# Kernel optimization log

Measured on AMD Instinct MI355X. Metric: run time of the kernel, lower is better.

Reference implementation:

```python
import jax, jax.numpy as jnp
import numpy as np

B, C, H, W = 16, 64, 64, 64
HW = H * W            # = dim = 4096
R = 4                 # reduction_ratio
NH = 8                # head_num
EPS = 1e-5


def setup_inputs() -> dict:
    key = jax.random.key(0)
    ks = jax.random.split(key, 8)
    s = 0.02  # weight init scale
    return {
        "x": jax.random.normal(ks[0], (B, C, H, W), jnp.float32),
        "ln1_w": jnp.ones((C,), jnp.float32),
        "ln1_b": jnp.zeros((C,), jnp.float32),
        "ln2_w": jnp.ones((C,), jnp.float32),
        "ln2_b": jnp.zeros((C,), jnp.float32),
        "W_rk": jax.random.normal(ks[1], (C * R, C), jnp.float32) * s,
        "W_rv": jax.random.normal(ks[2], (C * R, C), jnp.float32) * s,
        "W_q": jax.random.normal(ks[3], (HW, HW), jnp.float32) * s,
        "W_k": jax.random.normal(ks[4], (HW // R, HW // R), jnp.float32) * s,
        "W_v": jax.random.normal(ks[5], (HW // R, HW // R), jnp.float32) * s,
        "W_o": jax.random.normal(ks[6], (HW, HW), jnp.float32) * s,
    }


def _ln(x, w, b):
    # LayerNorm over last axis
    mu = jnp.mean(x, axis=-1, keepdims=True)
    var = jnp.mean((x - mu) ** 2, axis=-1, keepdims=True)
    return (x - mu) / jnp.sqrt(var + EPS) * w + b


def reference(x, ln1_w, ln1_b, ln2_w, ln2_b, W_rk, W_rv, W_q, W_k, W_v, W_o):
    b, c, h, w = x.shape
    hw = h * w
    # ln1: LayerNorm2d == per-pixel LayerNorm over channels
    xn = _ln(x.transpose(0, 2, 3, 1), ln1_w, ln1_b)      # [B,H,W,C]
    xf = xn.reshape(b, hw, c)                            # [B,HW,C] (row-major HW)
    # K/V spatial reduction: 'a (cd r) b -> a cd (b r)'
    kv = xf.reshape(b, hw // R, R, c).transpose(0, 1, 3, 2).reshape(b, hw // R, c * R)
    k = _ln(kv @ W_rk, ln2_w, ln2_b)                     # [B,HW/R,C]
    v = _ln(kv @ W_rv, ln2_w, ln2_b)                     # [B,HW/R,C]
    # projections over the SPATIAL axis (dim = HW)
    q = xf.transpose(0, 2, 1) @ W_q                      # [B,C,HW]
    k = k.transpose(0, 2, 1) @ W_k                       # [B,C,HW/R]
    v = v.transpose(0, 2, 1) @ W_v                       # [B,C,HW/R]
    Lq = hw // NH
    Lk = (hw // R) // NH
    # split heads along spatial axis, attend over channel dim C
    qh = q.reshape(b, c, NH, Lq).transpose(0, 2, 3, 1)   # [B,h,Lq,C]
    kh = k.reshape(b, c, NH, Lk).transpose(0, 2, 3, 1)   # [B,h,Lk,C]
    vh = v.reshape(b, c, NH, Lk).transpose(0, 2, 3, 1)   # [B,h,Lk,C]
    scale = float(hw // NH) ** 0.5
    attn = jax.nn.softmax(jnp.einsum('bhqc,bhkc->bhqk', qh, kh) / scale, axis=-1)
    # dropout is identity at inference
    o = jnp.einsum('bhqk,bhkc->bhqc', attn, vh)          # [B,h,Lq,C]
    # concat_head: heads become outer blocks of the spatial axis
    o = o.transpose(0, 3, 1, 2).reshape(b, c, hw)        # [B,C,HW]
    o = o @ W_o                                          # [B,C,HW]
    return o.reshape(b, c, h, w) + x
```

## Files before the change

kernel.cpp:

```cpp
#include <hip/hip_runtime.h>

typedef unsigned short u16;
typedef unsigned int u32;
typedef __attribute__((ext_vector_type(8))) __bf16 bf16x8;
typedef __attribute__((ext_vector_type(4))) float f32x4;
typedef __attribute__((ext_vector_type(4))) unsigned int u32x4;

#define MFMA16(a, b, c) __builtin_amdgcn_mfma_f32_16x16x32_bf16((a), (b), (c), 0, 0, 0)

__device__ __forceinline__ u16 f2bf(float f) {
  unsigned u = __float_as_uint(f);
  u += 0x7FFFu + ((u >> 16) & 1u);
  return (u16)(u >> 16);
}

typedef __attribute__((address_space(1))) const unsigned char gU8;
typedef __attribute__((address_space(3))) unsigned char sU8;
__device__ __forceinline__ void gload16(const void* g, void* l) {
  __builtin_amdgcn_global_load_lds((gU8*)g, (sU8*)l, 16, 0, 0);
}

__device__ __forceinline__ void wt_body2(const float* __restrict__ W, u16* __restrict__ Wt,
                                         int K, int N, int bid, float* tile) {
  int ntn = N >> 6;
  int kt2 = bid / ntn, nt = bid % ntn;
  int t = threadIdx.x;
  const float* src = W + (size_t)kt2 * 128 * N + (size_t)nt * 64;
  f32x4 r[8];
#pragma unroll
  for (int i = 0; i < 8; ++i) {
    int idx = t + i * 256, row = idx >> 4, c4 = idx & 15;
    r[i] = *(const f32x4*)&src[(size_t)row * N + c4 * 4];
  }
#pragma unroll
  for (int i = 0; i < 8; ++i) {
    int idx = t + i * 256, row = idx >> 4, c4 = idx & 15;
#pragma unroll
    for (int j = 0; j < 4; ++j) tile[row * 65 + c4 * 4 + j] = r[i][j];
  }
  __syncthreads();
  u16* dst = Wt + (size_t)nt * 64 * K + (size_t)kt2 * 128;
  int g = t & 7, n0 = t >> 3;
#pragma unroll
  for (int i = 0; i < 2; ++i) {
    int n = n0 + i * 32;
    float v[16];
#pragma unroll
    for (int j = 0; j < 16; ++j) v[j] = tile[(g * 16 + j) * 65 + n];
    u32x4 pk0, pk1;
#pragma unroll
    for (int j = 0; j < 4; ++j) {
      pk0[j] = (u32)f2bf(v[2 * j]) | ((u32)f2bf(v[2 * j + 1]) << 16);
      pk1[j] = (u32)f2bf(v[8 + 2 * j]) | ((u32)f2bf(v[8 + 2 * j + 1]) << 16);
    }
    *(u32x4*)&dst[(size_t)n * K + g * 16] = pk0;
    *(u32x4*)&dst[(size_t)n * K + g * 16 + 8] = pk1;
  }
}

__device__ __forceinline__ void wperm_body(const float* __restrict__ Wrk, const float* __restrict__ Wrv,
                                           u16* __restrict__ Wtk, u16* __restrict__ Wtv, int bid) {
  int idx = bid * 256 + threadIdx.x;
  int cp = idx >> 8, f = idx & 255;
  int k = ((f & 63) << 2) | (f >> 6);
  Wtk[idx] = f2bf(Wrk[k * 64 + cp]);
  Wtv[idx] = f2bf(Wrv[k * 64 + cp]);
}

__device__ __forceinline__ void ln1_body(const float* __restrict__ x, const float* __restrict__ w,
                                         const float* __restrict__ bias, u16* __restrict__ xf_pc,
                                         u16* __restrict__ xfT, int bid, float* tile) {
  int b = bid >> 6, p0 = (bid & 63) << 6;
  int t = threadIdx.x;
  const float* xb = x + (size_t)b * 64 * 4096;
  f32x4 r[4];
#pragma unroll
  for (int i = 0; i < 4; ++i) {
    int idx = t + i * 256, c = idx >> 4, p4 = idx & 15;
    r[i] = *(const f32x4*)&xb[(size_t)c * 4096 + p0 + p4 * 4];
  }
#pragma unroll
  for (int i = 0; i < 4; ++i) {
    int idx = t + i * 256, c = idx >> 4, p4 = idx & 15;
#pragma unroll
    for (int j = 0; j < 4; ++j) tile[c * 65 + p4 * 4 + j] = r[i][j];
  }
  __syncthreads();
  int lane = t & 63, wvx = t >> 6;
  float gw = w[lane], gb = bias[lane];
#pragma unroll
  for (int pp = 0; pp < 16; pp += 2) {
    int p = wvx * 16 + pp;
    float v0 = tile[lane * 65 + p], v1 = tile[lane * 65 + p + 1];
    float s0 = v0, q0 = v0 * v0, s1 = v1, q1 = v1 * v1;
#pragma unroll
    for (int m = 1; m < 64; m <<= 1) {
      s0 += __shfl_xor(s0, m); q0 += __shfl_xor(q0, m);
      s1 += __shfl_xor(s1, m); q1 += __shfl_xor(q1, m);
    }
    float mu0 = s0 * (1.0f / 64.0f), var0 = q0 * (1.0f / 64.0f) - mu0 * mu0;
    float mu1 = s1 * (1.0f / 64.0f), var1 = q1 * (1.0f / 64.0f) - mu1 * mu1;
    tile[lane * 65 + p]     = (v0 - mu0) * rsqrtf(var0 + 1e-5f) * gw + gb;
    tile[lane * 65 + p + 1] = (v1 - mu1) * rsqrtf(var1 + 1e-5f) * gw + gb;
  }
  __syncthreads();
  u16* xfb = xf_pc + (size_t)b * 4096 * 64;
  u16* xtb = xfT + (size_t)b * 64 * 4096;
  int i0 = t >> 3, j8 = t & 7;
  float vc[2][8];
#pragma unroll
  for (int i = 0; i < 2; ++i)
#pragma unroll
    for (int j = 0; j < 8; ++j) vc[i][j] = tile[(j8 * 8 + j) * 65 + i0 + i * 32];
#pragma unroll
  for (int i = 0; i < 2; ++i) {
    u32x4 pk;
#pragma unroll
    for (int j = 0; j < 4; ++j)
      pk[j] = (u32)f2bf(vc[i][2 * j]) | ((u32)f2bf(vc[i][2 * j + 1]) << 16);
    *(u32x4*)&xfb[(size_t)(p0 + i0 + i * 32) * 64 + j8 * 8] = pk;
  }
  float vr[2][8];
#pragma unroll
  for (int i = 0; i < 2; ++i)
#pragma unroll
    for (int j = 0; j < 8; ++j) vr[i][j] = tile[(i0 + i * 32) * 65 + j8 * 8 + j];
#pragma unroll
  for (int i = 0; i < 2; ++i) {
    u32x4 pk;
#pragma unroll
    for (int j = 0; j < 4; ++j)
      pk[j] = (u32)f2bf(vr[i][2 * j]) | ((u32)f2bf(vr[i][2 * j + 1]) << 16);
    *(u32x4*)&xtb[(size_t)(i0 + i * 32) * 4096 + p0 + j8 * 8] = pk;
  }
}

__global__ __launch_bounds__(256) void prep_kernel(
    const float* __restrict__ W_q, u16* __restrict__ Wt_q,
    const float* __restrict__ W_o, u16* __restrict__ Wt_o,
    const float* __restrict__ W_k, u16* __restrict__ Wt_k,
    const float* __restrict__ W_v, u16* __restrict__ Wt_v,
    const float* __restrict__ W_rk, const float* __restrict__ W_rv,
    u16* __restrict__ Wt_rk, u16* __restrict__ Wt_rv,
    const float* __restrict__ x, const float* __restrict__ ln1w, const float* __restrict__ ln1b,
    u16* __restrict__ xf_pc, u16* __restrict__ xfT) {
  __shared__ float tile[128 * 65];
  int bid = blockIdx.x;
  if (bid < 2048)       wt_body2(W_q, Wt_q, 4096, 4096, bid, tile);
  else if (bid < 4096)  wt_body2(W_o, Wt_o, 4096, 4096, bid - 2048, tile);
  else if (bid < 4224)  wt_body2(W_k, Wt_k, 1024, 1024, bid - 4096, tile);
  else if (bid < 4352)  wt_body2(W_v, Wt_v, 1024, 1024, bid - 4224, tile);
  else if (bid < 4416)  wperm_body(W_rk, W_rv, Wt_rk, Wt_rv, bid - 4352);
  else                  ln1_body(x, ln1w, ln1b, xf_pc, xfT, bid - 4416, tile);
}

__global__ __launch_bounds__(256) void kv_kernel(const u16* __restrict__ xf_pc,
                                                 const u16* __restrict__ Wtk, const u16* __restrict__ Wtv,
                                                 const float* __restrict__ ln2w, const float* __restrict__ ln2b,
                                                 u16* __restrict__ kT, u16* __restrict__ vT) {
  __shared__ __align__(16) u16 As[64 * 264];
  __shared__ __align__(16) u16 Bk[64 * 264];
  __shared__ __align__(16) u16 Bv[64 * 264];
  u16* Tk = As;
  u16* Tv = As + 64 * 72;
  int b = blockIdx.x >> 4, s0 = (blockIdx.x & 15) << 6;
  int t = threadIdx.x;
  const u16* Asrc = xf_pc + (size_t)b * 4096 * 64 + (size_t)s0 * 256;
#pragma unroll
  for (int i = 0; i < 8; ++i) {
    int id = t + i * 256, row = id >> 5, c16 = id & 31;
    *(u32x4*)&As[row * 264 + c16 * 8] = *(const u32x4*)&Asrc[(size_t)row * 256 + c16 * 8];
    *(u32x4*)&Bk[row * 264 + c16 * 8] = *(const u32x4*)&Wtk[(size_t)row * 256 + c16 * 8];
    *(u32x4*)&Bv[row * 264 + c16 * 8] = *(const u32x4*)&Wtv[(size_t)row * 256 + c16 * 8];
  }
  __syncthreads();
  int lane = t & 63, wv = t >> 6, lo = lane & 15, hi = lane >> 4;
  f32x4 acck[4] = {}, accv[4] = {};
  int arow = (wv * 16 + lo) * 264 + hi * 8;
#pragma unroll
  for (int kk = 0; kk < 8; ++kk) {
    bf16x8 a = *(const bf16x8*)&As[arow + kk * 32];
#pragma unroll
    for (int nf = 0; nf < 4; ++nf) {
      bf16x8 bk = *(const bf16x8*)&Bk[(nf * 16 + lo) * 264 + kk * 32 + hi * 8];
      bf16x8 bv = *(const bf16x8*)&Bv[(nf * 16 + lo) * 264 + kk * 32 + hi * 8];
      acck[nf] = MFMA16(a, bk, acck[nf]);
      accv[nf] = MFMA16(a, bv, accv[nf]);
    }
  }
  __syncthreads();
  float w2[4], b2[4];
#pragma unroll
  for (int nf = 0; nf < 4; ++nf) { w2[nf] = ln2w[nf * 16 + lo]; b2[nf] = ln2b[nf * 16 + lo]; }
#pragma unroll
  for (int r = 0; r < 4; ++r) {
    float sk = 0.f, sk2 = 0.f, sv = 0.f, sv2 = 0.f;
#pragma unroll
    for (int nf = 0; nf < 4; ++nf) {
      float a = acck[nf][r], c = accv[nf][r];
      sk += a; sk2 += a * a; sv += c; sv2 += c * c;
    }
#pragma unroll
    for (int m = 1; m < 16; m <<= 1) {
      sk += __shfl_xor(sk, m); sk2 += __shfl_xor(sk2, m);
      sv += __shfl_xor(sv, m); sv2 += __shfl_xor(sv2, m);
    }
    float mk = sk * (1.f / 64.f), vk = sk2 * (1.f / 64.f) - mk * mk, rk = rsqrtf(vk + 1e-5f);
    float mv = sv * (1.f / 64.f), vv = sv2 * (1.f / 64.f) - mv * mv, rv = rsqrtf(vv + 1e-5f);
    int srow = wv * 16 + hi * 4 + r;
#pragma unroll
    for (int nf = 0; nf < 4; ++nf) {
      Tk[(nf * 16 + lo) * 72 + srow] = f2bf((acck[nf][r] - mk) * rk * w2[nf] + b2[nf]);
      Tv[(nf * 16 + lo) * 72 + srow] = f2bf((accv[nf][r] - mv) * rv * w2[nf] + b2[nf]);
    }
  }
  __syncthreads();
  u16* kdst = kT + (size_t)b * 64 * 1024 + s0;
  u16* vdst = vT + (size_t)b * 64 * 1024 + s0;
#pragma unroll
  for (int i = 0; i < 16; ++i) {
    int idx = t + i * 256, cp = idx >> 6, s = idx & 63;
    kdst[(size_t)cp * 1024 + s] = Tk[cp * 72 + s];
    vdst[(size_t)cp * 1024 + s] = Tv[cp * 72 + s];
  }
}

__device__ __forceinline__ void stage32(const u16* Ab, const u16* Bb, int K, int kt,
                                        u16* As, u16* Bs, int wv, int lane) {
#pragma unroll
  for (int i = 0; i < 2; ++i) {
    int cb = wv * 2 + i;
    int c = cb * 64 + lane;
    int row = c >> 2, s = c & 3;
    int scol = (s ^ (row & 3)) << 3;
    gload16(Ab + (size_t)row * K + kt * 32 + scol, As + cb * 512);
    gload16(Bb + (size_t)row * K + kt * 32 + scol, Bs + cb * 512);
  }
}

__device__ __forceinline__ void compute32(const u16* As, const u16* Bs, f32x4 acc[4][4],
                                          int wm, int wn, int lo, int hi) {
  int slot = (hi ^ (lo & 3)) << 3;
  bf16x8 a[4], bb[4];
#pragma unroll
  for (int i = 0; i < 4; ++i) {
    a[i]  = *(const bf16x8*)&As[(wm + i * 16 + lo) * 32 + slot];
    bb[i] = *(const bf16x8*)&Bs[(wn + i * 16 + lo) * 32 + slot];
  }
#pragma unroll
  for (int mi = 0; mi < 4; ++mi)
#pragma unroll
    for (int ni = 0; ni < 4; ++ni)
      acc[mi][ni] = MFMA16(a[mi], bb[ni], acc[mi][ni]);
}

template <int EPI>
__device__ void gemm_body(const u16* __restrict__ A, const u16* __restrict__ Bm,
                          u16* __restrict__ Cc, int N, int K, int chunkStride,
                          int mt, int nt, int koff, int nk, u16* lds) {
  int t = threadIdx.x, lane = t & 63, wv = t >> 6;
  int wm = (wv >> 1) * 64, wn = (wv & 1) * 64;
  int lo = lane & 15, hi = lane >> 4;
  f32x4 acc[4][4] = {};
  const u16* Ab = A + (size_t)mt * 128 * K + koff;
  const u16* Bb = Bm + (size_t)nt * 128 * K + koff;
  u16* bufs[3] = {lds, lds + 8192, lds + 16384};
  stage32(Ab, Bb, K, 0, bufs[0], bufs[0] + 4096, wv, lane);
  stage32(Ab, Bb, K, 1, bufs[1], bufs[1] + 4096, wv, lane);
  for (int kt = 0; kt < nk; ++kt) {
    if (kt + 1 < nk) asm volatile("s_waitcnt vmcnt(4)" ::: "memory");
    else             asm volatile("s_waitcnt vmcnt(0)" ::: "memory");
    __builtin_amdgcn_s_barrier();
    __builtin_amdgcn_sched_barrier(0);
    if (kt + 2 < nk) {
      u16* nb = bufs[(kt + 2) % 3];
      stage32(Ab, Bb, K, kt + 2, nb, nb + 4096, wv, lane);
    }
    u16* cb = bufs[kt % 3];
    compute32(cb, cb + 4096, acc, wm, wn, lo, hi);
  }
#pragma unroll
  for (int mi = 0; mi < 4; ++mi)
#pragma unroll
    for (int ni = 0; ni < 4; ++ni)
#pragma unroll
      for (int r = 0; r < 4; ++r) {
        int m = mt * 128 + wm + mi * 16 + hi * 4 + r;
        int n = nt * 128 + wn + ni * 16 + lo;
        float v = acc[mi][ni][r];
        if constexpr (EPI == 0) {
          Cc[(size_t)m * N + n] = f2bf(v);
        } else {
          Cc[(size_t)(n >> 6) * chunkStride + (size_t)m * 64 + (n & 63)] = f2bf(v);
        }
      }
}

__global__ __launch_bounds__(256, 3) void qkv_kernel(
    const u16* __restrict__ Wt_q, const u16* __restrict__ xfT, u16* __restrict__ q_t,
    const u16* __restrict__ Wt_k, const u16* __restrict__ k_lnT, u16* __restrict__ kproj,
    const u16* __restrict__ v_lnT, const u16* __restrict__ Wt_v, u16* __restrict__ vproj) {
  __shared__ __align__(16) u16 lds[24576];
  int bid = blockIdx.x;
  if (bid < 1024) {
    int log = (bid & 7) * 128 + (bid >> 3);
    int kh = log >> 8, tile = log & 255, mt = tile >> 3, nt = tile & 7;
    gemm_body<1>(Wt_q, xfT, q_t + (size_t)kh * 4194304, 1024, 4096, 4096 * 64,
                 mt, nt, kh * 1024, 32, lds);
  } else if (bid < 1088) {
    int id = bid - 1024;
    gemm_body<1>(Wt_k, k_lnT, kproj, 1024, 1024, 1024 * 64, id >> 3, id & 7, 0, 32, lds);
  } else {
    int id = bid - 1088;
    gemm_body<0>(v_lnT, Wt_v, vproj, 1024, 1024, 0, id >> 3, id & 7, 0, 32, lds);
  }
}

__global__ __launch_bounds__(256, 3) void ogemm_kernel(const u16* __restrict__ o2,
                                                       const u16* __restrict__ Wt_o,
                                                       u16* __restrict__ o_part) {
  __shared__ __align__(16) u16 lds[24576];
  int bid = blockIdx.x;
  int log = (bid & 7) * 64 + (bid >> 3);
  int kh = log >> 8, tile = log & 255, mt = tile >> 5, nt = tile & 31;
  gemm_body<0>(o2, Wt_o, o_part + (size_t)kh * 4194304, 4096, 4096, 0,
               mt, nt, kh * 2048, 64, lds);
}

__global__ __launch_bounds__(256) void oreduce_kernel(const float* __restrict__ x,
                                                      const u16* __restrict__ p0,
                                                      const u16* __restrict__ p1,
                                                      float* __restrict__ out) {
  size_t base = ((size_t)blockIdx.x * 256 + threadIdx.x) * 8;
  u32x4 a = *(const u32x4*)&p0[base];
  u32x4 b = *(const u32x4*)&p1[base];
  f32x4 x0 = *(const f32x4*)&x[base];
  f32x4 x1 = *(const f32x4*)&x[base + 4];
  float r[8];
#pragma unroll
  for (int j = 0; j < 4; ++j) {
    r[2 * j]     = __uint_as_float(a[j] << 16) + __uint_as_float(b[j] << 16);
    r[2 * j + 1] = __uint_as_float(a[j] & 0xFFFF0000u) + __uint_as_float(b[j] & 0xFFFF0000u);
  }
  f32x4 o0, o1;
#pragma unroll
  for (int j = 0; j < 4; ++j) { o0[j] = r[j] + x0[j]; o1[j] = r[4 + j] + x1[j]; }
  *(f32x4*)&out[base] = o0;
  *(f32x4*)&out[base + 4] = o1;
}

__global__ __launch_bounds__(256) void attn_kernel(const u16* __restrict__ qp, const u16* __restrict__ kp,
                                                   const u16* __restrict__ vp, u16* __restrict__ o2) {
  __shared__ __align__(16) u16 Qs[128 * 72];
  __shared__ __align__(16) u16 Ks[128 * 72];
  __shared__ __align__(16) u16 Vs[64 * 136];
  __shared__ __align__(16) u16 Ps[128 * 136];
  int qt = blockIdx.x & 3, h = (blockIdx.x >> 2) & 7, b = blockIdx.x >> 5;
  int t = threadIdx.x, lane = t & 63, wv = t >> 6;
  int lo = lane & 15, hi = lane >> 4;
  const u16* qsrc = qp + (size_t)b * 262144 + (size_t)(h * 512 + qt * 128) * 64;
  const u16* ksrc = kp + (size_t)b * 1024 * 64 + (size_t)(h * 128) * 64;
  const u16* vsrc = vp + (size_t)b * 64 * 1024 + h * 128;
#pragma unroll
  for (int i = 0; i < 4; ++i) {
    int id = t + i * 256, row = id >> 3, c8 = id & 7;
    size_t goff = (size_t)row * 64 + c8 * 8;
    float f[8] = {0.f, 0.f, 0.f, 0.f, 0.f, 0.f, 0.f, 0.f};
#pragma unroll
    for (int kh = 0; kh < 4; ++kh) {
      u32x4 pk = *(const u32x4*)&qsrc[(size_t)kh * 4194304 + goff];
#pragma unroll
      for (int j = 0; j < 4; ++j) {
        f[2 * j]     += __uint_as_float(pk[j] << 16);
        f[2 * j + 1] += __uint_as_float(pk[j] & 0xFFFF0000u);
      }
    }
    u32x4 pko;
#pragma unroll
    for (int j = 0; j < 4; ++j) pko[j] = (u32)f2bf(f[2 * j]) | ((u32)f2bf(f[2 * j + 1]) << 16);
    *(u32x4*)&Qs[row * 72 + c8 * 8] = pko;
  }
#pragma unroll
  for (int i = 0; i < 4; ++i) {
    int id = t + i * 256;
    int row = id >> 3, c16 = id & 7;
    *(u32x4*)&Ks[row * 72 + c16 * 8] = *(const u32x4*)&ksrc[(size_t)row * 64 + c16 * 8];
    int vrow = id >> 4, v16 = id & 15;
    *(u32x4*)&Vs[vrow * 136 + v16 * 8] = *(const u32x4*)&vsrc[(size_t)vrow * 1024 + v16 * 8];
  }
  __syncthreads();
  f32x4 s[2][8] = {};
#pragma unroll
  for (int kk = 0; kk < 2; ++kk) {
    bf16x8 a0 = *(const bf16x8*)&Qs[(wv * 32 + lo) * 72 + kk * 32 + hi * 8];
    bf16x8 a1 = *(const bf16x8*)&Qs[(wv * 32 + 16 + lo) * 72 + kk * 32 + hi * 8];
#pragma unroll
    for (int ni = 0; ni < 8; ++ni) {
      bf16x8 bb = *(const bf16x8*)&Ks[(ni * 16 + lo) * 72 + kk * 32 + hi * 8];
      s[0][ni] = MFMA16(a0, bb, s[0][ni]);
      s[1][ni] = MFMA16(a1, bb, s[1][ni]);
    }
  }
  const float inv_scale = 0.044194173824159216f;
#pragma unroll
  for (int mi = 0; mi < 2; ++mi)
#pragma unroll
    for (int ni = 0; ni < 8; ++ni) s[mi][ni] *= inv_scale;
#pragma unroll
  for (int mi = 0; mi < 2; ++mi) {
#pragma unroll
    for (int r = 0; r < 4; ++r) {
      float mx = -1e30f;
#pragma unroll
      for (int ni = 0; ni < 8; ++ni) mx = fmaxf(mx, s[mi][ni][r]);
#pragma unroll
      for (int m = 1; m < 16; m <<= 1) mx = fmaxf(mx, __shfl_xor(mx, m));
      float p[8], sum = 0.f;
#pragma unroll
      for (int ni = 0; ni < 8; ++ni) { p[ni] = __expf(s[mi][ni][r] - mx); sum += p[ni]; }
#pragma unroll
      for (int m = 1; m < 16; m <<= 1) sum += __shfl_xor(sum, m);
      float rs = 1.0f / sum;
      int row = wv * 32 + mi * 16 + hi * 4 + r;
#pragma unroll
      for (int ni = 0; ni < 8; ++ni) Ps[row * 136 + ni * 16 + lo] = f2bf(p[ni] * rs);
    }
  }
  __syncthreads();
  f32x4 o[4][2] = {};
#pragma unroll
  for (int kk = 0; kk < 4; ++kk) {
    bf16x8 b0 = *(const bf16x8*)&Ps[(wv * 32 + lo) * 136 + kk * 32 + hi * 8];
    bf16x8 b1 = *(const bf16x8*)&Ps[(wv * 32 + 16 + lo) * 136 + kk * 32 + hi * 8];
#pragma unroll
    for (int mi = 0; mi < 4; ++mi) {
      bf16x8 a = *(const bf16x8*)&Vs[(mi * 16 + lo) * 136 + kk * 32 + hi * 8];
      o[mi][0] = MFMA16(a, b0, o[mi][0]);
      o[mi][1] = MFMA16(a, b1, o[mi][1]);
    }
  }
  u16* od = o2 + (size_t)b * 64 * 4096 + h * 512 + qt * 128;
#pragma unroll
  for (int mi = 0; mi < 4; ++mi)
#pragma unroll
    for (int ni = 0; ni < 2; ++ni)
#pragma unroll
      for (int r = 0; r < 4; ++r) {
        int c = mi * 16 + hi * 4 + r;
        int lq = wv * 32 + ni * 16 + lo;
        od[(size_t)c * 4096 + lq] = f2bf(o[mi][ni][r]);
      }
}

extern "C" void kernel_launch(void* const* d_in, const int* in_sizes, int n_in,
                              void* d_out, int out_size, void* d_ws, size_t ws_size,
                              hipStream_t stream) {
  (void)in_sizes; (void)n_in; (void)out_size; (void)ws_size;
  const float* x    = (const float*)d_in[0];
  const float* ln1w = (const float*)d_in[1];
  const float* ln1b = (const float*)d_in[2];
  const float* ln2w = (const float*)d_in[3];
  const float* ln2b = (const float*)d_in[4];
  const float* W_rk = (const float*)d_in[5];
  const float* W_rv = (const float*)d_in[6];
  const float* W_q  = (const float*)d_in[7];
  const float* W_k  = (const float*)d_in[8];
  const float* W_v  = (const float*)d_in[9];
  const float* W_o  = (const float*)d_in[10];

  char* ws = (char*)d_ws;
  size_t off = 0;
  auto alloc = [&](size_t bytes) { char* p = ws + off; off += bytes; return p; };
  u16* Wt_q  = (u16*)alloc(4096ull * 4096 * 2);
  u16* Wt_o  = (u16*)alloc(4096ull * 4096 * 2);
  u16* Wt_k  = (u16*)alloc(1024ull * 1024 * 2);
  u16* Wt_v  = (u16*)alloc(1024ull * 1024 * 2);
  u16* Wt_rk = (u16*)alloc(64ull * 256 * 2);
  u16* Wt_rv = (u16*)alloc(64ull * 256 * 2);
  u16* xf_pc = (u16*)alloc(16ull * 4096 * 64 * 2);
  u16* xfT   = (u16*)alloc(16ull * 64 * 4096 * 2);
  u16* k_lnT = (u16*)alloc(16ull * 64 * 1024 * 2);
  u16* v_lnT = (u16*)alloc(16ull * 64 * 1024 * 2);
  u16* q_t   = (u16*)alloc(4ull * 16 * 4096 * 64 * 2);
  u16* kproj = (u16*)alloc(16ull * 1024 * 64 * 2);
  u16* vproj = (u16*)alloc(16ull * 64 * 1024 * 2);
  u16* o2     = xfT;
  u16* o_part = Wt_q;

  prep_kernel<<<5440, 256, 0, stream>>>(W_q, Wt_q, W_o, Wt_o, W_k, Wt_k, W_v, Wt_v,
                                        W_rk, W_rv, Wt_rk, Wt_rv, x, ln1w, ln1b, xf_pc, xfT);
  kv_kernel<<<256, 256, 0, stream>>>(xf_pc, Wt_rk, Wt_rv, ln2w, ln2b, k_lnT, v_lnT);
  qkv_kernel<<<1152, 256, 0, stream>>>(Wt_q, xfT, q_t, Wt_k, k_lnT, kproj, v_lnT, Wt_v, vproj);
  attn_kernel<<<512, 256, 0, stream>>>(q_t, kproj, vproj, o2);
  ogemm_kernel<<<512, 256, 0, stream>>>(o2, Wt_o, o_part);
  oreduce_kernel<<<2048, 256, 0, stream>>>(x, o_part, o_part + 4194304, (float*)d_out);
}
```

Measured before the change: 211.6 us.

## Redistribute weight transpose/convert work into later kernels to overlap with GEMMs

```diff
diff --git a/kernel.cpp b/kernel.cpp
--- a/kernel.cpp
+++ b/kernel.cpp
@@ -137,9 +137,6 @@
 
 __global__ __launch_bounds__(256) void prep_kernel(
     const float* __restrict__ W_q, u16* __restrict__ Wt_q,
-    const float* __restrict__ W_o, u16* __restrict__ Wt_o,
-    const float* __restrict__ W_k, u16* __restrict__ Wt_k,
-    const float* __restrict__ W_v, u16* __restrict__ Wt_v,
     const float* __restrict__ W_rk, const float* __restrict__ W_rv,
     u16* __restrict__ Wt_rk, u16* __restrict__ Wt_rv,
     const float* __restrict__ x, const float* __restrict__ ln1w, const float* __restrict__ ln1b,
@@ -147,23 +144,29 @@
   __shared__ float tile[128 * 65];
   int bid = blockIdx.x;
   if (bid < 2048)       wt_body2(W_q, Wt_q, 4096, 4096, bid, tile);
-  else if (bid < 4096)  wt_body2(W_o, Wt_o, 4096, 4096, bid - 2048, tile);
-  else if (bid < 4224)  wt_body2(W_k, Wt_k, 1024, 1024, bid - 4096, tile);
-  else if (bid < 4352)  wt_body2(W_v, Wt_v, 1024, 1024, bid - 4224, tile);
-  else if (bid < 4416)  wperm_body(W_rk, W_rv, Wt_rk, Wt_rv, bid - 4352);
-  else                  ln1_body(x, ln1w, ln1b, xf_pc, xfT, bid - 4416, tile);
+  else if (bid < 2112)  wperm_body(W_rk, W_rv, Wt_rk, Wt_rv, bid - 2048);
+  else                  ln1_body(x, ln1w, ln1b, xf_pc, xfT, bid - 2112, tile);
 }
 
 __global__ __launch_bounds__(256) void kv_kernel(const u16* __restrict__ xf_pc,
                                                  const u16* __restrict__ Wtk, const u16* __restrict__ Wtv,
                                                  const float* __restrict__ ln2w, const float* __restrict__ ln2b,
-                                                 u16* __restrict__ kT, u16* __restrict__ vT) {
+                                                 u16* __restrict__ kT, u16* __restrict__ vT,
+                                                 const float* __restrict__ W_k, u16* __restrict__ Wt_k,
+                                                 const float* __restrict__ W_v, u16* __restrict__ Wt_v) {
   __shared__ __align__(16) u16 As[64 * 264];
   __shared__ __align__(16) u16 Bk[64 * 264];
   __shared__ __align__(16) u16 Bv[64 * 264];
+  int bid0 = blockIdx.x;
+  if (bid0 >= 256) {
+    int id = bid0 - 256;
+    if (id < 128) wt_body2(W_k, Wt_k, 1024, 1024, id, (float*)As);
+    else          wt_body2(W_v, Wt_v, 1024, 1024, id - 128, (float*)As);
+    return;
+  }
   u16* Tk = As;
   u16* Tv = As + 64 * 72;
-  int b = blockIdx.x >> 4, s0 = (blockIdx.x & 15) << 6;
+  int b = bid0 >> 4, s0 = (bid0 & 15) << 6;
   int t = threadIdx.x;
   const u16* Asrc = xf_pc + (size_t)b * 4096 * 64 + (size_t)s0 * 256;
 #pragma unroll
@@ -299,7 +302,8 @@
 __global__ __launch_bounds__(256, 3) void qkv_kernel(
     const u16* __restrict__ Wt_q, const u16* __restrict__ xfT, u16* __restrict__ q_t,
     const u16* __restrict__ Wt_k, const u16* __restrict__ k_lnT, u16* __restrict__ kproj,
-    const u16* __restrict__ v_lnT, const u16* __restrict__ Wt_v, u16* __restrict__ vproj) {
+    const u16* __restrict__ v_lnT, const u16* __restrict__ Wt_v, u16* __restrict__ vproj,
+    const float* __restrict__ W_o, u16* __restrict__ Wt_o) {
   __shared__ __align__(16) u16 lds[24576];
   int bid = blockIdx.x;
   if (bid < 1024) {
@@ -310,9 +314,11 @@
   } else if (bid < 1088) {
     int id = bid - 1024;
     gemm_body<1>(Wt_k, k_lnT, kproj, 1024, 1024, 1024 * 64, id >> 3, id & 7, 0, 32, lds);
-  } else {
+  } else if (bid < 1152) {
     int id = bid - 1088;
     gemm_body<0>(v_lnT, Wt_v, vproj, 1024, 1024, 0, id >> 3, id & 7, 0, 32, lds);
+  } else {
+    wt_body2(W_o, Wt_o, 4096, 4096, bid - 1152, (float*)lds);
   }
 }
 
@@ -487,10 +493,12 @@
   u16* o2     = xfT;
   u16* o_part = Wt_q;
 
-  prep_kernel<<<5440, 256, 0, stream>>>(W_q, Wt_q, W_o, Wt_o, W_k, Wt_k, W_v, Wt_v,
-                                        W_rk, W_rv, Wt_rk, Wt_rv, x, ln1w, ln1b, xf_pc, xfT);
-  kv_kernel<<<256, 256, 0, stream>>>(xf_pc, Wt_rk, Wt_rv, ln2w, ln2b, k_lnT, v_lnT);
-  qkv_kernel<<<1152, 256, 0, stream>>>(Wt_q, xfT, q_t, Wt_k, k_lnT, kproj, v_lnT, Wt_v, vproj);
+  prep_kernel<<<3136, 256, 0, stream>>>(W_q, Wt_q, W_rk, W_rv, Wt_rk, Wt_rv,
+                                        x, ln1w, ln1b, xf_pc, xfT);
+  kv_kernel<<<512, 256, 0, stream>>>(xf_pc, Wt_rk, Wt_rv, ln2w, ln2b, k_lnT, v_lnT,
+                                     W_k, Wt_k, W_v, Wt_v);
+  qkv_kernel<<<3200, 256, 0, stream>>>(Wt_q, xfT, q_t, Wt_k, k_lnT, kproj, v_lnT, Wt_v, vproj,
+                                       W_o, Wt_o);
   attn_kernel<<<512, 256, 0, stream>>>(q_t, kproj, vproj, o2);
   ogemm_kernel<<<512, 256, 0, stream>>>(o2, Wt_o, o_part);
   oreduce_kernel<<<2048, 256, 0, stream>>>(x, o_part, o_part + 4194304, (float*)d_out);
```

New measurement: 210.8 us. About the same (-0.3%).

## Remove split-K from Q and output GEMMs, fuse residual into epilogue

Applied to the files above, without the earlier changes.

```diff
diff --git a/kernel.cpp b/kernel.cpp
--- a/kernel.cpp
+++ b/kernel.cpp
@@ -256,14 +256,14 @@
 
 template <int EPI>
 __device__ void gemm_body(const u16* __restrict__ A, const u16* __restrict__ Bm,
-                          u16* __restrict__ Cc, int N, int K, int chunkStride,
-                          int mt, int nt, int koff, int nk, u16* lds) {
+                          void* __restrict__ Cc, const float* __restrict__ resid,
+                          int N, int K, int chunkStride, int mt, int nt, int nk, u16* lds) {
   int t = threadIdx.x, lane = t & 63, wv = t >> 6;
   int wm = (wv >> 1) * 64, wn = (wv & 1) * 64;
   int lo = lane & 15, hi = lane >> 4;
   f32x4 acc[4][4] = {};
-  const u16* Ab = A + (size_t)mt * 128 * K + koff;
-  const u16* Bb = Bm + (size_t)nt * 128 * K + koff;
+  const u16* Ab = A + (size_t)mt * 128 * K;
+  const u16* Bb = Bm + (size_t)nt * 128 * K;
   u16* bufs[3] = {lds, lds + 8192, lds + 16384};
   stage32(Ab, Bb, K, 0, bufs[0], bufs[0] + 4096, wv, lane);
   stage32(Ab, Bb, K, 1, bufs[1], bufs[1] + 4096, wv, lane);
@@ -289,9 +289,12 @@
         int n = nt * 128 + wn + ni * 16 + lo;
         float v = acc[mi][ni][r];
         if constexpr (EPI == 0) {
-          Cc[(size_t)m * N + n] = f2bf(v);
+          ((u16*)Cc)[(size_t)m * N + n] = f2bf(v);
+        } else if constexpr (EPI == 1) {
+          ((u16*)Cc)[(size_t)(n >> 6) * chunkStride + (size_t)m * 64 + (n & 63)] = f2bf(v);
         } else {
-          Cc[(size_t)(n >> 6) * chunkStride + (size_t)m * 64 + (n & 63)] = f2bf(v);
+          size_t ad = (size_t)m * N + n;
+          ((float*)Cc)[ad] = v + resid[ad];
         }
       }
 }
@@ -302,51 +305,24 @@
     const u16* __restrict__ v_lnT, const u16* __restrict__ Wt_v, u16* __restrict__ vproj) {
   __shared__ __align__(16) u16 lds[24576];
   int bid = blockIdx.x;
-  if (bid < 1024) {
-    int log = (bid & 7) * 128 + (bid >> 3);
-    int kh = log >> 8, tile = log & 255, mt = tile >> 3, nt = tile & 7;
-    gemm_body<1>(Wt_q, xfT, q_t + (size_t)kh * 4194304, 1024, 4096, 4096 * 64,
-                 mt, nt, kh * 1024, 32, lds);
-  } else if (bid < 1088) {
-    int id = bid - 1024;
-    gemm_body<1>(Wt_k, k_lnT, kproj, 1024, 1024, 1024 * 64, id >> 3, id & 7, 0, 32, lds);
+  if (bid < 256) {
+    gemm_body<1>(Wt_q, xfT, q_t, nullptr, 1024, 4096, 4096 * 64, bid >> 3, bid & 7, 128, lds);
+  } else if (bid < 320) {
+    int id = bid - 256;
+    gemm_body<1>(Wt_k, k_lnT, kproj, nullptr, 1024, 1024, 1024 * 64, id >> 3, id & 7, 32, lds);
   } else {
-    int id = bid - 1088;
-    gemm_body<0>(v_lnT, Wt_v, vproj, 1024, 1024, 0, id >> 3, id & 7, 0, 32, lds);
+    int id = bid - 320;
+    gemm_body<0>(v_lnT, Wt_v, vproj, nullptr, 1024, 1024, 0, id >> 3, id & 7, 32, lds);
   }
 }
 
 __global__ __launch_bounds__(256, 3) void ogemm_kernel(const u16* __restrict__ o2,
                                                        const u16* __restrict__ Wt_o,
-                                                       u16* __restrict__ o_part) {
+                                                       float* __restrict__ out,
+                                                       const float* __restrict__ x) {
   __shared__ __align__(16) u16 lds[24576];
   int bid = blockIdx.x;
-  int log = (bid & 7) * 64 + (bid >> 3);
-  int kh = log >> 8, tile = log & 255, mt = tile >> 5, nt = tile & 31;
-  gemm_body<0>(o2, Wt_o, o_part + (size_t)kh * 4194304, 4096, 4096, 0,
-               mt, nt, kh * 2048, 64, lds);
-}
-
-__global__ __launch_bounds__(256) void oreduce_kernel(const float* __restrict__ x,
-                                                      const u16* __restrict__ p0,
-                                                      const u16* __restrict__ p1,
-                                                      float* __restrict__ out) {
-  size_t base = ((size_t)blockIdx.x * 256 + threadIdx.x) * 8;
-  u32x4 a = *(const u32x4*)&p0[base];
-  u32x4 b = *(const u32x4*)&p1[base];
-  f32x4 x0 = *(const f32x4*)&x[base];
-  f32x4 x1 = *(const f32x4*)&x[base + 4];
-  float r[8];
-#pragma unroll
-  for (int j = 0; j < 4; ++j) {
-    r[2 * j]     = __uint_as_float(a[j] << 16) + __uint_as_float(b[j] << 16);
-    r[2 * j + 1] = __uint_as_float(a[j] & 0xFFFF0000u) + __uint_as_float(b[j] & 0xFFFF0000u);
-  }
-  f32x4 o0, o1;
-#pragma unroll
-  for (int j = 0; j < 4; ++j) { o0[j] = r[j] + x0[j]; o1[j] = r[4 + j] + x1[j]; }
-  *(f32x4*)&out[base] = o0;
-  *(f32x4*)&out[base + 4] = o1;
+  gemm_body<2>(o2, Wt_o, out, x, 4096, 4096, 0, bid >> 5, bid & 31, 128, lds);
 }
 
 __global__ __launch_bounds__(256) void attn_kernel(const u16* __restrict__ qp, const u16* __restrict__ kp,
@@ -363,27 +339,9 @@
   const u16* vsrc = vp + (size_t)b * 64 * 1024 + h * 128;
 #pragma unroll
   for (int i = 0; i < 4; ++i) {
-    int id = t + i * 256, row = id >> 3, c8 = id & 7;
-    size_t goff = (size_t)row * 64 + c8 * 8;
-    float f[8] = {0.f, 0.f, 0.f, 0.f, 0.f, 0.f, 0.f, 0.f};
-#pragma unroll
-    for (int kh = 0; kh < 4; ++kh) {
-      u32x4 pk = *(const u32x4*)&qsrc[(size_t)kh * 4194304 + goff];
-#pragma unroll
-      for (int j = 0; j < 4; ++j) {
-        f[2 * j]     += __uint_as_float(pk[j] << 16);
-        f[2 * j + 1] += __uint_as_float(pk[j] & 0xFFFF0000u);
-      }
-    }
-    u32x4 pko;
-#pragma unroll
-    for (int j = 0; j < 4; ++j) pko[j] = (u32)f2bf(f[2 * j]) | ((u32)f2bf(f[2 * j + 1]) << 16);
-    *(u32x4*)&Qs[row * 72 + c8 * 8] = pko;
-  }
-#pragma unroll
-  for (int i = 0; i < 4; ++i) {
     int id = t + i * 256;
     int row = id >> 3, c16 = id & 7;
+    *(u32x4*)&Qs[row * 72 + c16 * 8] = *(const u32x4*)&qsrc[(size_t)row * 64 + c16 * 8];
     *(u32x4*)&Ks[row * 72 + c16 * 8] = *(const u32x4*)&ksrc[(size_t)row * 64 + c16 * 8];
     int vrow = id >> 4, v16 = id & 15;
     *(u32x4*)&Vs[vrow * 136 + v16 * 8] = *(const u32x4*)&vsrc[(size_t)vrow * 1024 + v16 * 8];
@@ -481,17 +439,15 @@
   u16* xfT   = (u16*)alloc(16ull * 64 * 4096 * 2);
   u16* k_lnT = (u16*)alloc(16ull * 64 * 1024 * 2);
   u16* v_lnT = (u16*)alloc(16ull * 64 * 1024 * 2);
-  u16* q_t   = (u16*)alloc(4ull * 16 * 4096 * 64 * 2);
+  u16* q_t   = (u16*)alloc(16ull * 4096 * 64 * 2);
   u16* kproj = (u16*)alloc(16ull * 1024 * 64 * 2);
   u16* vproj = (u16*)alloc(16ull * 64 * 1024 * 2);
-  u16* o2     = xfT;
-  u16* o_part = Wt_q;
+  u16* o2    = xfT;
 
   prep_kernel<<<5440, 256, 0, stream>>>(W_q, Wt_q, W_o, Wt_o, W_k, Wt_k, W_v, Wt_v,
                                         W_rk, W_rv, Wt_rk, Wt_rv, x, ln1w, ln1b, xf_pc, xfT);
   kv_kernel<<<256, 256, 0, stream>>>(xf_pc, Wt_rk, Wt_rv, ln2w, ln2b, k_lnT, v_lnT);
-  qkv_kernel<<<1152, 256, 0, stream>>>(Wt_q, xfT, q_t, Wt_k, k_lnT, kproj, v_lnT, Wt_v, vproj);
+  qkv_kernel<<<384, 256, 0, stream>>>(Wt_q, xfT, q_t, Wt_k, k_lnT, kproj, v_lnT, Wt_v, vproj);
   attn_kernel<<<512, 256, 0, stream>>>(q_t, kproj, vproj, o2);
-  ogemm_kernel<<<512, 256, 0, stream>>>(o2, Wt_o, o_part);
-  oreduce_kernel<<<2048, 256, 0, stream>>>(x, o_part, o_part + 4194304, (float*)d_out);
-}
+  ogemm_kernel<<<256, 256, 0, stream>>>(o2, Wt_o, (float*)d_out, x);
+}
```

Result: slower. 246.4 us (+16.4%).
